# Performance work log

Measured on AMD Instinct MI355X. Metric: run time of the kernel, lower is better.

## Reference

```python
import jax, jax.numpy as jnp
import numpy as np

HIDDEN = 2048
HEADS = 16
HEAD_DIM = HIDDEN // HEADS  # 128
B, S = 2, 2048
SCALE = 1.0 / np.sqrt(HEAD_DIM)


def setup_inputs() -> dict:
    key = jax.random.key(0)
    ks = jax.random.split(key, 9)
    x = jax.random.normal(ks[0], (B, S, HIDDEN), dtype=jnp.float32)
    # causal mask, broadcastable to [B, 1(group), H, S, S]
    mask = jnp.tril(jnp.ones((S, S), dtype=bool))[None, None, None, :, :]
    mask = jnp.broadcast_to(mask, (B, 1, 1, S, S))
    s = 0.02
    Wq = jax.random.normal(ks[1], (HIDDEN, HIDDEN), dtype=jnp.float32) * s
    bq = jnp.zeros((HIDDEN,), dtype=jnp.float32)
    Wk = jax.random.normal(ks[2], (HIDDEN, HEAD_DIM), dtype=jnp.float32) * s
    bk = jnp.zeros((HEAD_DIM,), dtype=jnp.float32)
    Wv = jax.random.normal(ks[3], (HIDDEN, HEAD_DIM), dtype=jnp.float32) * s
    bv = jnp.zeros((HEAD_DIM,), dtype=jnp.float32)
    Wo = jax.random.normal(ks[4], (HIDDEN, HIDDEN), dtype=jnp.float32) * s
    bo = jnp.zeros((HIDDEN,), dtype=jnp.float32)
    return {"x": x, "mask": mask, "Wq": Wq, "bq": bq, "Wk": Wk, "bk": bk,
            "Wv": Wv, "bv": bv, "Wo": Wo, "bo": bo}


def reference(x, mask, Wq, bq, Wk, bk, Wv, bv, Wo, bo):
    b, s, _ = x.shape
    q = (x @ Wq + bq).reshape(b, s, HEADS, HEAD_DIM)   # [b,s,h,d]
    k = x @ Wk + bk                                    # [b,t,d] single shared KV head
    v = x @ Wv + bv                                    # [b,t,d]
    # scores: [b, h, s, t]; add group dim to match mask [b,1,h,s,t]
    scores = jnp.einsum('bshd,btd->bhst', q, k) * SCALE
    scores = scores[:, None]                            # [b,1,h,s,t]
    scores = jnp.where(mask, scores, jnp.float32(-jnp.inf))
    att = jax.nn.softmax(scores, axis=-1)[:, 0]         # [b,h,s,t] (dropout eval = identity)
    out = jnp.einsum('bhst,btd->bshd', att, v).reshape(b, s, HIDDEN)
    return out @ Wo + bo
```

## Files before the change

### kernel.cpp

```cpp
#include <hip/hip_runtime.h>


#define HIDDEN 2048
#define NHEADS 16
#define HDIM 128
#define BATCH 2
#define SEQ 2048
#define SCALE_L2E 0.1275258653864023f

typedef __attribute__((ext_vector_type(8))) short bfrag;
typedef __attribute__((ext_vector_type(4))) float facc;
typedef __attribute__((ext_vector_type(4))) unsigned int uifrag;

__device__ __forceinline__ unsigned short f2bf(float f) {
  unsigned int u = __float_as_uint(f);
  u += 0x7fffu + ((u >> 16) & 1u);
  return (unsigned short)(u >> 16);
}

__device__ __forceinline__ unsigned int cvt_pk_bf16(float lo, float hi) {
  unsigned int r;
  asm("v_cvt_pk_bf16_f32 %0, %1, %2" : "=v"(r) : "v"(lo), "v"(hi));
  return r;
}

__device__ __forceinline__ void gl_lds16(const void* g, void* l) {
  __builtin_amdgcn_global_load_lds(
      (const __attribute__((address_space(1))) void*)g,
      (__attribute__((address_space(3))) void*)l, 16, 0, 0);
}

#define SBAR() __builtin_amdgcn_s_barrier()
#define CFENCE() asm volatile("" ::: "memory")
#define WAIT_VM(n) asm volatile("s_waitcnt vmcnt(" #n ")" ::: "memory")

__global__ __launch_bounds__(256) void cvt_bf16(const float* __restrict__ in,
                                                unsigned int* __restrict__ out, int n4) {
  int i = blockIdx.x * 256 + threadIdx.x;
  if (i >= n4) return;
  float4 v = ((const float4*)in)[i];
  uint2 o = {cvt_pk_bf16(v.x, v.y), cvt_pk_bf16(v.z, v.w)};
  ((uint2*)out)[i] = o;
}

__global__ __launch_bounds__(256) void transpose_cvt2(const float* __restrict__ W0,
                                                      short* __restrict__ T0,
                                                      const float* __restrict__ W1,
                                                      short* __restrict__ T1,
                                                      int K, int N,
                                                      float s0, float s1) {
  const float* W = blockIdx.z ? W1 : W0;
  short* WT = blockIdx.z ? T1 : T0;
  const float s = blockIdx.z ? s1 : s0;
  __shared__ float t[32][33];
  int tx = threadIdx.x & 31, ty = threadIdx.x >> 5;
  int n0 = blockIdx.x * 32, k0 = blockIdx.y * 32;
#pragma unroll
  for (int j = 0; j < 4; ++j)
    t[ty + j * 8][tx] = W[(size_t)(k0 + ty + j * 8) * N + n0 + tx];
  __syncthreads();
#pragma unroll
  for (int j = 0; j < 4; ++j)
    WT[(size_t)(n0 + ty + j * 8) * K + k0 + tx] = (short)f2bf(t[tx][ty + j * 8] * s);
}

#define GEMM_STAGE8(buf, kt)                                                   \
  _Pragma("unroll") for (int it_ = 0; it_ < 2; ++it_) {                        \
    gl_lds16(ap[it_] + (kt) * 64, &Al[buf][(w * 2 + it_) * 512]);              \
    gl_lds16(bp[it_] + (kt) * 64, &Bl[buf][(w * 2 + it_) * 512]);              \
  }

#define GEMM_PIPE_LOOP8(A, BT, Kdim)                                           \
  facc acc[2][4] = {};                                                         \
  const int nkt = (Kdim) >> 6;                                                 \
  const short *ap[2], *bp[2];                                                  \
  _Pragma("unroll") for (int it_ = 0; it_ < 2; ++it_) {                        \
    int C = (w * 2 + it_) * 64 + l;                                            \
    int row = C >> 3, c = C & 7;                                               \
    int sz = (c ^ (row & 7)) << 3;                                             \
    ap[it_] = (A) + (size_t)(m0 + row) * (Kdim) + sz;                          \
    bp[it_] = (BT) + (size_t)(n0 + row) * (Kdim) + sz;                         \
  }                                                                            \
  int aoffs[2][2], boffs[2][4];                                                \
  _Pragma("unroll") for (int ks = 0; ks < 2; ++ks) {                           \
    _Pragma("unroll") for (int mt = 0; mt < 2; ++mt) {                         \
      int row = wm * 32 + mt * 16 + l15, c = ks * 4 + l4;                      \
      aoffs[ks][mt] = row * 128 + ((c ^ (row & 7)) << 4);                      \
    }                                                                          \
    _Pragma("unroll") for (int nt = 0; nt < 4; ++nt) {                         \
      int row = wn * 64 + nt * 16 + l15, c = ks * 4 + l4;                      \
      boffs[ks][nt] = row * 128 + ((c ^ (row & 7)) << 4);                      \
    }                                                                          \
  }                                                                            \
  GEMM_STAGE8(0, 0)                                                            \
  for (int kt = 0; kt < nkt; ++kt) {                                           \
    const int cur = kt & 1;                                                    \
    if (kt + 1 < nkt) {                                                        \
      GEMM_STAGE8(cur ^ 1, kt + 1)                                             \
      WAIT_VM(4);                                                              \
    } else {                                                                   \
      WAIT_VM(0);                                                              \
    }                                                                          \
    SBAR();                                                                    \
    CFENCE();                                                                  \
    const char* AlB = (const char*)Al + (cur << 14);                           \
    const char* BlB = (const char*)Bl + (cur << 14);                           \
    __builtin_amdgcn_s_setprio(1);                                             \
    _Pragma("unroll") for (int ks = 0; ks < 2; ++ks) {                         \
      bfrag af[2], bf[4];                                                      \
      _Pragma("unroll") for (int mt = 0; mt < 2; ++mt)                         \
        af[mt] = *(const bfrag*)(AlB + aoffs[ks][mt]);                         \
      _Pragma("unroll") for (int nt = 0; nt < 4; ++nt)                         \
        bf[nt] = *(const bfrag*)(BlB + boffs[ks][nt]);                         \
      _Pragma("unroll") for (int mt = 0; mt < 2; ++mt)                         \
          _Pragma("unroll") for (int nt = 0; nt < 4; ++nt)                     \
              acc[mt][nt] = __builtin_amdgcn_mfma_f32_16x16x32_bf16(           \
                  af[mt], bf[nt], acc[mt][nt], 0, 0, 0);                       \
    }                                                                          \
    __builtin_amdgcn_s_setprio(0);                                             \
    CFENCE();                                                                  \
    SBAR();                                                                    \
    CFENCE();                                                                  \
  }

__device__ __forceinline__ int pv_perm64(int row) {
  int k = row & 63;
  int p = (k & 0x23) | ((k & 0x0C) << 1) | ((k & 0x10) >> 2);
  return (row & ~63) | p;
}

__global__ __launch_bounds__(512, 4) void gemm_qkv(const short* __restrict__ A,
                                                   const short* __restrict__ BT,
                                                   const float* __restrict__ bq,
                                                   const float* __restrict__ bk,
                                                   const float* __restrict__ bv,
                                                   unsigned short* __restrict__ Qb,
                                                   unsigned short* __restrict__ Kb,
                                                   unsigned short* __restrict__ Vtb,
                                                   int M, int K) {
  __shared__ __align__(16) short Al[2][128 * 64];
  __shared__ __align__(16) short Bl[2][128 * 64];
  const int tid = threadIdx.x;
  const int w = tid >> 6, l = tid & 63;
  const int wm = w >> 1, wn = w & 1;
  const int l15 = l & 15, l4 = l >> 4;
  const int m0 = blockIdx.x * 128, n0 = blockIdx.y * 128;
  GEMM_PIPE_LOOP8(A, BT, K)
#pragma unroll
  for (int mt = 0; mt < 2; ++mt) {
#pragma unroll
    for (int nt = 0; nt < 4; ++nt) {
#pragma unroll
      for (int r = 0; r < 4; ++r) {
        int row = m0 + wm * 32 + mt * 16 + l4 * 4 + r;
        int col = n0 + wn * 64 + nt * 16 + l15;
        float v = acc[mt][nt][r];
        if (col < HIDDEN) {
          Qb[(size_t)row * HIDDEN + col] = f2bf(v + bq[col] * SCALE_L2E);
        } else if (col < HIDDEN + HDIM) {
          int lc = col - HIDDEN;
          Kb[(size_t)row * HDIM + lc] = f2bf(v + bk[lc]);
        } else {
          int lc = col - HIDDEN - HDIM;
          Vtb[(size_t)lc * M + pv_perm64(row)] = f2bf(v + bv[lc]);
        }
      }
    }
  }
}

__global__ __launch_bounds__(512, 4) void gemm_out(const short* __restrict__ A,
                                                   const short* __restrict__ BT,
                                                   const float* __restrict__ bias,
                                                   float* __restrict__ Cout,
                                                   int M, int N, int K) {
  __shared__ __align__(16) short Al[2][128 * 64];
  __shared__ __align__(16) short Bl[2][128 * 64];
  const int tid = threadIdx.x;
  const int w = tid >> 6, l = tid & 63;
  const int wm = w >> 1, wn = w & 1;
  const int l15 = l & 15, l4 = l >> 4;
  const int m0 = blockIdx.x * 128, n0 = blockIdx.y * 128;
  GEMM_PIPE_LOOP8(A, BT, K)
#pragma unroll
  for (int mt = 0; mt < 2; ++mt)
#pragma unroll
    for (int nt = 0; nt < 4; ++nt)
#pragma unroll
      for (int r = 0; r < 4; ++r) {
        int row = m0 + wm * 32 + mt * 16 + l4 * 4 + r;
        int col = n0 + wn * 64 + nt * 16 + l15;
        Cout[(size_t)row * N + col] = acc[mt][nt][r] + bias[col];
      }
}

__global__ __launch_bounds__(256, 2) void attn_kernel(const short* __restrict__ Q,
                                                      const short* __restrict__ Kg,
                                                      const short* __restrict__ Vt,
                                                      unsigned short* __restrict__ O) {
  __shared__ __align__(16) short Kl[2][64 * 128];
  __shared__ __align__(16) short Vl[2][128 * 64];
  const int tid = threadIdx.x;
  const int w = tid >> 6, l = tid & 63;
  const int l15 = l & 15, l4 = l >> 4;
  const int h = blockIdx.y, b = blockIdx.z;

  int kgo[4], vgo[4];
#pragma unroll
  for (int it = 0; it < 4; ++it) {
    int C = (w * 4 + it) * 64 + l;
    int key = C >> 4, ck = C & 15;
    kgo[it] = key * HDIM + ((ck ^ (key & 7)) << 3);
    int d = C >> 3, cv = C & 7;
    vgo[it] = d * (BATCH * SEQ) + ((cv ^ (d & 7)) << 3);
  }
  int koffs[16], voffs[16];
#pragma unroll
  for (int kk = 0; kk < 4; ++kk)
#pragma unroll
    for (int kt = 0; kt < 4; ++kt) {
      int key = kt * 16 + l15, c = kk * 4 + l4;
      koffs[kk * 4 + kt] = key * 256 + ((c ^ (key & 7)) << 4);
    }
#pragma unroll
  for (int c = 0; c < 2; ++c)
#pragma unroll
    for (int nt = 0; nt < 8; ++nt) {
      int d = nt * 16 + l15, cc = c * 4 + l4;
      voffs[c * 8 + nt] = d * 128 + ((cc ^ (d & 7)) << 4);
    }
  const short* kg0 = Kg + (size_t)b * SEQ * HDIM;
  const short* vg0 = Vt + (size_t)b * SEQ;

#define STAGE_KV(buf, t)                                                       \
  do {                                                                         \
    const short* kgp = kg0 + (size_t)(t) * (64 * HDIM);                        \
    const short* vgp = vg0 + (size_t)(t) * 64;                                 \
    _Pragma("unroll") for (int it = 0; it < 4; ++it)                           \
        gl_lds16(kgp + kgo[it], &Kl[buf][(w * 4 + it) * 512]);                 \
    _Pragma("unroll") for (int it = 0; it < 4; ++it)                           \
        gl_lds16(vgp + vgo[it], &Vl[buf][(w * 4 + it) * 512]);                 \
  } while (0)

  for (int pass = 0; pass < 2; ++pass) {
    const int qtile = (pass == 0) ? (int)blockIdx.x : 31 - (int)blockIdx.x;
    const int q0 = qtile * 64;
    const int qw = q0 + w * 16;

    bfrag aq[4];
#pragma unroll
    for (int kk = 0; kk < 4; ++kk)
      aq[kk] = *(const bfrag*)(Q + (size_t)(b * SEQ + qw + l15) * HIDDEN +
                               h * HDIM + kk * 32 + l4 * 8);

    facc accO[8] = {};
    float mrow = -INFINITY, lrow = 0.f;
    const int nkv = qtile + 1;

    STAGE_KV(0, 0);

    for (int t = 0; t < nkv; ++t) {
      const int cur = t & 1;
      if (t + 1 < nkv) {
        STAGE_KV(cur ^ 1, t + 1);
        WAIT_VM(8);
      } else {
        WAIT_VM(0);
      }
      SBAR();
      CFENCE();
      const int kv0 = t << 6;
      const char* KlB = (const char*)Kl + (cur << 14);
      const char* VlB = (const char*)Vl + (cur << 14);

      facc sac[4] = {};
      __builtin_amdgcn_s_setprio(1);
#pragma unroll
      for (int kk = 0; kk < 4; ++kk) {
#pragma unroll
        for (int kt = 0; kt < 4; ++kt) {
          bfrag ak = *(const bfrag*)(KlB + koffs[kk * 4 + kt]);
          sac[kt] = __builtin_amdgcn_mfma_f32_16x16x32_bf16(ak, aq[kk], sac[kt], 0, 0, 0);
        }
      }
      __builtin_amdgcn_s_setprio(0);

      bfrag bv[16];
#pragma unroll
      for (int i = 0; i < 16; ++i)
        bv[i] = *(const bfrag*)(VlB + voffs[i]);
      CFENCE();
      SBAR();
      CFENCE();

      const int qg = qw + l15;
      const bool needmask = (kv0 + 63 > qw);
      float p[4][4];
#pragma unroll
      for (int kt = 0; kt < 4; ++kt)
#pragma unroll
        for (int r = 0; r < 4; ++r) {
          float v = sac[kt][r];
          if (needmask) {
            int keyg = kv0 + kt * 16 + l4 * 4 + r;
            v = (keyg <= qg) ? v : -INFINITY;
          }
          p[kt][r] = v;
        }
      float m0_ = fmaxf(fmaxf(p[0][0], p[0][1]), fmaxf(p[0][2], p[0][3]));
      float m1_ = fmaxf(fmaxf(p[1][0], p[1][1]), fmaxf(p[1][2], p[1][3]));
      float m2_ = fmaxf(fmaxf(p[2][0], p[2][1]), fmaxf(p[2][2], p[2][3]));
      float m3_ = fmaxf(fmaxf(p[3][0], p[3][1]), fmaxf(p[3][2], p[3][3]));
      float mt = fmaxf(fmaxf(m0_, m1_), fmaxf(m2_, m3_));
      mt = fmaxf(mt, __shfl_xor(mt, 16));
      mt = fmaxf(mt, __shfl_xor(mt, 32));
      if (!__all(mt <= mrow + 8.0f)) {
        float mn = fmaxf(mrow, mt);
        float f = exp2f(mrow - mn);
        mrow = mn;
        lrow *= f;
        float fr[4];
#pragma unroll
        for (int r = 0; r < 4; ++r) fr[r] = __shfl(f, l4 * 4 + r);
#pragma unroll
        for (int nt = 0; nt < 8; ++nt)
#pragma unroll
          for (int r = 0; r < 4; ++r) accO[nt][r] *= fr[r];
      }
#pragma unroll
      for (int kt = 0; kt < 4; ++kt)
#pragma unroll
        for (int r = 0; r < 4; ++r) p[kt][r] = exp2f(p[kt][r] - mrow);
      float s0_ = (p[0][0] + p[0][1]) + (p[0][2] + p[0][3]);
      float s1_ = (p[1][0] + p[1][1]) + (p[1][2] + p[1][3]);
      float s2_ = (p[2][0] + p[2][1]) + (p[2][2] + p[2][3]);
      float s3_ = (p[3][0] + p[3][1]) + (p[3][2] + p[3][3]);
      float ps = (s0_ + s1_) + (s2_ + s3_);
      ps += __shfl_xor(ps, 16);
      ps += __shfl_xor(ps, 32);
      lrow += ps;

      __builtin_amdgcn_s_setprio(1);
#pragma unroll
      for (int c = 0; c < 2; ++c) {
        uifrag up;
        up.x = cvt_pk_bf16(p[2 * c][0], p[2 * c][1]);
        up.y = cvt_pk_bf16(p[2 * c][2], p[2 * c][3]);
        up.z = cvt_pk_bf16(p[2 * c + 1][0], p[2 * c + 1][1]);
        up.w = cvt_pk_bf16(p[2 * c + 1][2], p[2 * c + 1][3]);
        bfrag pa = __builtin_bit_cast(bfrag, up);
#pragma unroll
        for (int nt = 0; nt < 8; ++nt)
          accO[nt] = __builtin_amdgcn_mfma_f32_16x16x32_bf16(pa, bv[c * 8 + nt],
                                                             accO[nt], 0, 0, 0);
      }
      __builtin_amdgcn_s_setprio(0);
    }

    float inv = 1.f / lrow;
#pragma unroll
    for (int r = 0; r < 4; ++r) {
      float invr = __shfl(inv, l4 * 4 + r);
      int row = qw + l4 * 4 + r;
#pragma unroll
      for (int nt = 0; nt < 8; ++nt)
        O[(size_t)(b * SEQ + row) * HIDDEN + h * HDIM + nt * 16 + l15] =
            f2bf(accO[nt][r] * invr);
    }
  }
#undef STAGE_KV
}

extern "C" void kernel_launch(void* const* d_in, const int* in_sizes, int n_in,
                              void* d_out, int out_size, void* d_ws, size_t ws_size,
                              hipStream_t stream) {
  const float* x = (const float*)d_in[0];
  const float* Wq = (const float*)d_in[2];
  const float* bq = (const float*)d_in[3];
  const float* Wk = (const float*)d_in[4];
  const float* bk = (const float*)d_in[5];
  const float* Wv = (const float*)d_in[6];
  const float* bv = (const float*)d_in[7];
  const float* Wo = (const float*)d_in[8];
  const float* bo = (const float*)d_in[9];
  float* out = (float*)d_out;

  const size_t MS = (size_t)BATCH * SEQ;
  char* ws = (char*)d_ws;
  short* xb = (short*)ws;      ws += MS * HIDDEN * 2;
  short* WqkvT = (short*)ws;   ws += (size_t)(HIDDEN + 2 * HDIM) * HIDDEN * 2;
  short* WoT = (short*)ws;     ws += (size_t)HIDDEN * HIDDEN * 2;
  short* Qb = (short*)ws;      ws += MS * HIDDEN * 2;
  short* Kb = (short*)ws;      ws += MS * HDIM * 2;
  short* Vtb = (short*)ws;     ws += (size_t)HDIM * MS * 2;
  short* Ab = (short*)ws;      ws += MS * HIDDEN * 2;

  cvt_bf16<<<(int)(MS * HIDDEN / 4 / 256), 256, 0, stream>>>(
      x, (unsigned int*)xb, (int)(MS * HIDDEN / 4));
  transpose_cvt2<<<dim3(HIDDEN / 32, HIDDEN / 32, 2), 256, 0, stream>>>(
      Wq, WqkvT, Wo, WoT, HIDDEN, HIDDEN, SCALE_L2E, 1.0f);
  transpose_cvt2<<<dim3(HDIM / 32, HIDDEN / 32, 2), 256, 0, stream>>>(
      Wk, WqkvT + (size_t)HIDDEN * HIDDEN, Wv, WqkvT + (size_t)(HIDDEN + HDIM) * HIDDEN,
      HIDDEN, HDIM, 1.0f, 1.0f);

  gemm_qkv<<<dim3(32, 18), 512, 0, stream>>>(xb, WqkvT, bq, bk, bv,
                                             (unsigned short*)Qb, (unsigned short*)Kb,
                                             (unsigned short*)Vtb, (int)MS, HIDDEN);

  attn_kernel<<<dim3(16, NHEADS, BATCH), 256, 0, stream>>>(Qb, Kb, Vtb,
                                                           (unsigned short*)Ab);

  gemm_out<<<dim3(32, 16), 512, 0, stream>>>(Ab, WoT, bo, out, (int)MS, HIDDEN, HIDDEN);
}
```

Measured before the change: 203.1 us.

## Process two 16-row query subtiles per wave in attention to reuse K/V fragments

Each wave now computes 32 query rows instead of 16, so every K fragment loaded from LDS feeds two score MFMAs and every V fragment feeds two PV MFMAs. Query tiles grow to 128 rows, the grid halves, and launch bounds drop to one block per CU to allow the doubled accumulator registers. This cuts LDS traffic and barrier overhead per FLOP. The cost is lower occupancy and fewer blocks for latency hiding and load balance.

```diff
diff --git a/kernel.cpp b/kernel.cpp
--- a/kernel.cpp
+++ b/kernel.cpp
@@ -194,7 +194,7 @@
       }
 }
 
-__global__ __launch_bounds__(256, 2) void attn_kernel(const short* __restrict__ Q,
+__global__ __launch_bounds__(256, 1) void attn_kernel(const short* __restrict__ Q,
                                                       const short* __restrict__ Kg,
                                                       const short* __restrict__ Vt,
                                                       unsigned short* __restrict__ O) {
@@ -243,19 +243,21 @@
   } while (0)
 
   for (int pass = 0; pass < 2; ++pass) {
-    const int qtile = (pass == 0) ? (int)blockIdx.x : 31 - (int)blockIdx.x;
-    const int q0 = qtile * 64;
-    const int qw = q0 + w * 16;
-
-    bfrag aq[4];
-#pragma unroll
-    for (int kk = 0; kk < 4; ++kk)
-      aq[kk] = *(const bfrag*)(Q + (size_t)(b * SEQ + qw + l15) * HIDDEN +
-                               h * HDIM + kk * 32 + l4 * 8);
-
-    facc accO[8] = {};
-    float mrow = -INFINITY, lrow = 0.f;
-    const int nkv = qtile + 1;
+    const int qtile = (pass == 0) ? (int)blockIdx.x : 15 - (int)blockIdx.x;
+    const int q0 = qtile * 128;
+    const int qw = q0 + w * 32;
+
+    bfrag aq[2][4];
+#pragma unroll
+    for (int s = 0; s < 2; ++s)
+#pragma unroll
+      for (int kk = 0; kk < 4; ++kk)
+        aq[s][kk] = *(const bfrag*)(Q + (size_t)(b * SEQ + qw + s * 16 + l15) * HIDDEN +
+                                    h * HDIM + kk * 32 + l4 * 8);
+
+    facc accO[2][8] = {};
+    float mrow[2] = {-INFINITY, -INFINITY}, lrow[2] = {0.f, 0.f};
+    const int nkv = 2 * qtile + 2;
 
     STAGE_KV(0, 0);
 
@@ -273,14 +275,15 @@
       const char* KlB = (const char*)Kl + (cur << 14);
       const char* VlB = (const char*)Vl + (cur << 14);
 
-      facc sac[4] = {};
+      facc sac[2][4] = {};
       __builtin_amdgcn_s_setprio(1);
 #pragma unroll
       for (int kk = 0; kk < 4; ++kk) {
 #pragma unroll
         for (int kt = 0; kt < 4; ++kt) {
           bfrag ak = *(const bfrag*)(KlB + koffs[kk * 4 + kt]);
-          sac[kt] = __builtin_amdgcn_mfma_f32_16x16x32_bf16(ak, aq[kk], sac[kt], 0, 0, 0);
+          sac[0][kt] = __builtin_amdgcn_mfma_f32_16x16x32_bf16(ak, aq[0][kk], sac[0][kt], 0, 0, 0);
+          sac[1][kt] = __builtin_amdgcn_mfma_f32_16x16x32_bf16(ak, aq[1][kk], sac[1][kt], 0, 0, 0);
         }
       }
       __builtin_amdgcn_s_setprio(0);
@@ -293,79 +296,94 @@
       SBAR();
       CFENCE();
 
-      const int qg = qw + l15;
-      const bool needmask = (kv0 + 63 > qw);
-      float p[4][4];
-#pragma unroll
-      for (int kt = 0; kt < 4; ++kt)
-#pragma unroll
-        for (int r = 0; r < 4; ++r) {
-          float v = sac[kt][r];
-          if (needmask) {
-            int keyg = kv0 + kt * 16 + l4 * 4 + r;
-            v = (keyg <= qg) ? v : -INFINITY;
+      unsigned int u[2][8];
+#pragma unroll
+      for (int s = 0; s < 2; ++s) {
+        const int qg = qw + s * 16 + l15;
+        const bool needmask = (kv0 + 63 > qw + s * 16);
+        float p[4][4];
+#pragma unroll
+        for (int kt = 0; kt < 4; ++kt)
+#pragma unroll
+          for (int r = 0; r < 4; ++r) {
+            float v = sac[s][kt][r];
+            if (needmask) {
+              int keyg = kv0 + kt * 16 + l4 * 4 + r;
+              v = (keyg <= qg) ? v : -INFINITY;
+            }
+            p[kt][r] = v;
           }
-          p[kt][r] = v;
+        float m0_ = fmaxf(fmaxf(p[0][0], p[0][1]), fmaxf(p[0][2], p[0][3]));
+        float m1_ = fmaxf(fmaxf(p[1][0], p[1][1]), fmaxf(p[1][2], p[1][3]));
+        float m2_ = fmaxf(fmaxf(p[2][0], p[2][1]), fmaxf(p[2][2], p[2][3]));
+        float m3_ = fmaxf(fmaxf(p[3][0], p[3][1]), fmaxf(p[3][2], p[3][3]));
+        float mt = fmaxf(fmaxf(m0_, m1_), fmaxf(m2_, m3_));
+        mt = fmaxf(mt, __shfl_xor(mt, 16));
+        mt = fmaxf(mt, __shfl_xor(mt, 32));
+        if (!__all(mt <= mrow[s] + 8.0f)) {
+          float mn = fmaxf(mrow[s], mt);
+          float f = exp2f(mrow[s] - mn);
+          mrow[s] = mn;
+          lrow[s] *= f;
+          float fr[4];
+#pragma unroll
+          for (int r = 0; r < 4; ++r) fr[r] = __shfl(f, l4 * 4 + r);
+#pragma unroll
+          for (int nt = 0; nt < 8; ++nt)
+#pragma unroll
+            for (int r = 0; r < 4; ++r) accO[s][nt][r] *= fr[r];
         }
-      float m0_ = fmaxf(fmaxf(p[0][0], p[0][1]), fmaxf(p[0][2], p[0][3]));
-      float m1_ = fmaxf(fmaxf(p[1][0], p[1][1]), fmaxf(p[1][2], p[1][3]));
-      float m2_ = fmaxf(fmaxf(p[2][0], p[2][1]), fmaxf(p[2][2], p[2][3]));
-      float m3_ = fmaxf(fmaxf(p[3][0], p[3][1]), fmaxf(p[3][2], p[3][3]));
-      float mt = fmaxf(fmaxf(m0_, m1_), fmaxf(m2_, m3_));
-      mt = fmaxf(mt, __shfl_xor(mt, 16));
-      mt = fmaxf(mt, __shfl_xor(mt, 32));
-      if (!__all(mt <= mrow + 8.0f)) {
-        float mn = fmaxf(mrow, mt);
-        float f = exp2f(mrow - mn);
-        mrow = mn;
-        lrow *= f;
-        float fr[4];
-#pragma unroll
-        for (int r = 0; r < 4; ++r) fr[r] = __shfl(f, l4 * 4 + r);
-#pragma unroll
-        for (int nt = 0; nt < 8; ++nt)
-#pragma unroll
-          for (int r = 0; r < 4; ++r) accO[nt][r] *= fr[r];
-      }
-#pragma unroll
-      for (int kt = 0; kt < 4; ++kt)
-#pragma unroll
-        for (int r = 0; r < 4; ++r) p[kt][r] = exp2f(p[kt][r] - mrow);
-      float s0_ = (p[0][0] + p[0][1]) + (p[0][2] + p[0][3]);
-      float s1_ = (p[1][0] + p[1][1]) + (p[1][2] + p[1][3]);
-      float s2_ = (p[2][0] + p[2][1]) + (p[2][2] + p[2][3]);
-      float s3_ = (p[3][0] + p[3][1]) + (p[3][2] + p[3][3]);
-      float ps = (s0_ + s1_) + (s2_ + s3_);
-      ps += __shfl_xor(ps, 16);
-      ps += __shfl_xor(ps, 32);
-      lrow += ps;
+#pragma unroll
+        for (int kt = 0; kt < 4; ++kt)
+#pragma unroll
+          for (int r = 0; r < 4; ++r) p[kt][r] = exp2f(p[kt][r] - mrow[s]);
+        float s0_ = (p[0][0] + p[0][1]) + (p[0][2] + p[0][3]);
+        float s1_ = (p[1][0] + p[1][1]) + (p[1][2] + p[1][3]);
+        float s2_ = (p[2][0] + p[2][1]) + (p[2][2] + p[2][3]);
+        float s3_ = (p[3][0] + p[3][1]) + (p[3][2] + p[3][3]);
+        float ps = (s0_ + s1_) + (s2_ + s3_);
+        ps += __shfl_xor(ps, 16);
+        ps += __shfl_xor(ps, 32);
+        lrow[s] += ps;
+#pragma unroll
+        for (int kt = 0; kt < 4; ++kt) {
+          u[s][kt * 2 + 0] = cvt_pk_bf16(p[kt][0], p[kt][1]);
+          u[s][kt * 2 + 1] = cvt_pk_bf16(p[kt][2], p[kt][3]);
+        }
+      }
 
       __builtin_amdgcn_s_setprio(1);
 #pragma unroll
       for (int c = 0; c < 2; ++c) {
-        uifrag up;
-        up.x = cvt_pk_bf16(p[2 * c][0], p[2 * c][1]);
-        up.y = cvt_pk_bf16(p[2 * c][2], p[2 * c][3]);
-        up.z = cvt_pk_bf16(p[2 * c + 1][0], p[2 * c + 1][1]);
-        up.w = cvt_pk_bf16(p[2 * c + 1][2], p[2 * c + 1][3]);
-        bfrag pa = __builtin_bit_cast(bfrag, up);
-#pragma unroll
-        for (int nt = 0; nt < 8; ++nt)
-          accO[nt] = __builtin_amdgcn_mfma_f32_16x16x32_bf16(pa, bv[c * 8 + nt],
-                                                             accO[nt], 0, 0, 0);
+#pragma unroll
+        for (int s = 0; s < 2; ++s) {
+          uifrag up;
+          up.x = u[s][c * 4 + 0];
+          up.y = u[s][c * 4 + 1];
+          up.z = u[s][c * 4 + 2];
+          up.w = u[s][c * 4 + 3];
+          bfrag pa = __builtin_bit_cast(bfrag, up);
+#pragma unroll
+          for (int nt = 0; nt < 8; ++nt)
+            accO[s][nt] = __builtin_amdgcn_mfma_f32_16x16x32_bf16(pa, bv[c * 8 + nt],
+                                                                  accO[s][nt], 0, 0, 0);
+        }
       }
       __builtin_amdgcn_s_setprio(0);
     }
 
-    float inv = 1.f / lrow;
-#pragma unroll
-    for (int r = 0; r < 4; ++r) {
-      float invr = __shfl(inv, l4 * 4 + r);
-      int row = qw + l4 * 4 + r;
-#pragma unroll
-      for (int nt = 0; nt < 8; ++nt)
-        O[(size_t)(b * SEQ + row) * HIDDEN + h * HDIM + nt * 16 + l15] =
-            f2bf(accO[nt][r] * invr);
+#pragma unroll
+    for (int s = 0; s < 2; ++s) {
+      float inv = 1.f / lrow[s];
+#pragma unroll
+      for (int r = 0; r < 4; ++r) {
+        float invr = __shfl(inv, l4 * 4 + r);
+        int row = qw + s * 16 + l4 * 4 + r;
+#pragma unroll
+        for (int nt = 0; nt < 8; ++nt)
+          O[(size_t)(b * SEQ + row) * HIDDEN + h * HDIM + nt * 16 + l15] =
+              f2bf(accO[s][nt][r] * invr);
+      }
     }
   }
 #undef STAGE_KV
@@ -407,8 +425,8 @@
                                              (unsigned short*)Qb, (unsigned short*)Kb,
                                              (unsigned short*)Vtb, (int)MS, HIDDEN);
 
-  attn_kernel<<<dim3(16, NHEADS, BATCH), 256, 0, stream>>>(Qb, Kb, Vtb,
-                                                           (unsigned short*)Ab);
+  attn_kernel<<<dim3(8, NHEADS, BATCH), 256, 0, stream>>>(Qb, Kb, Vtb,
+                                                          (unsigned short*)Ab);
 
   gemm_out<<<dim3(32, 16), 512, 0, stream>>>(Ab, WoT, bo, out, (int)MS, HIDDEN, HIDDEN);
 }
```

New measurement: 235.2 us. 15.8% more time.
